# Optimization experiments

Hardware: AMD Instinct MI355X
Metric: run time of the kernel (lower is better)

Reference implementation:

```python
import jax, jax.numpy as jnp
import numpy as np

EPS = 1e-6
MAX_Q = 25.0
B, M, N, S = 1024, 8192, 32, 128


def setup_inputs() -> dict:
    key = jax.random.key(0)
    k = jax.random.split(key, 6)
    z = jax.random.normal(k[0], (B, N), jnp.float32) * 1e-3
    z_j = jax.random.uniform(k[1], (M, N), jnp.float32, -1e-3, 1e-3)
    vec_d_j = jax.random.uniform(k[2], (M, N), jnp.float32, -1e-3, 1e-3)
    T_hat_j = jax.random.uniform(k[3], (M, S), jnp.float32, -1e-3, 1e-3)
    alpha_j = jnp.ones((M,), jnp.float32)
    sigma_par = jax.random.uniform(k[4], (M,), jnp.float32, 0.9, 1.5)
    sigma_perp = jax.random.uniform(k[5], (M,), jnp.float32, 0.1, 0.8)
    return {"z": z, "z_j": z_j, "vec_d_j": vec_d_j, "T_hat_j": T_hat_j,
            "alpha_j": alpha_j, "sigma_par": sigma_par, "sigma_perp": sigma_perp}


def reference(z, z_j, vec_d_j, T_hat_j, alpha_j, sigma_par, sigma_perp):
    tiny = jnp.finfo(sigma_par.dtype).eps
    w_par = 1.0 / jnp.maximum(sigma_par, tiny) ** 2      # [M]
    w_perp = 1.0 / jnp.maximum(sigma_perp, tiny) ** 2    # [M]
    w_diff = w_par - w_perp                               # [M]

    dz = z[:, None, :] - z_j[None, :, :]                  # [B, M, N]
    dz_norm_sq = jnp.sum(dz * dz, axis=-1)                # [B, M]

    d_norm = jnp.linalg.norm(vec_d_j, axis=-1, keepdims=True)  # [M, 1]
    use_proj = (d_norm > EPS).astype(z.dtype)                   # [M, 1]
    b = jnp.where(d_norm > EPS, vec_d_j / d_norm, jnp.zeros_like(vec_d_j))  # [M, N]
    proj = jnp.einsum('bmn,mn->bm', dz, b) * use_proj[:, 0][None, :]        # [B, M]

    q_pos = w_perp[None, :] * dz_norm_sq + w_diff[None, :] * (proj * proj)  # [B, M]
    q_pos = jnp.minimum(q_pos, jnp.asarray(MAX_Q, dtype=z.dtype))

    gain = alpha_j[None, :] * jnp.exp(-jnp.pi * q_pos)    # [B, M]
    T = gain @ T_hat_j                                     # [B, S]
    return T
```

## Files before the change

### kernel.cpp

```cpp
#include <hip/hip_runtime.h>
#include <hip/hip_bf16.h>
#include <math.h>

#define B_SZ 1024
#define M_SZ 8192
#define N_SZ 32
#define S_SZ 128

#define BT     32
#define NTHR   256
#define NSPLIT 16
#define MT     (M_SZ / NSPLIT)
#define MCH    256

#define SG_STRIDE 264

typedef __bf16 bf16x8 __attribute__((ext_vector_type(8)));
typedef float  f32x4  __attribute__((ext_vector_type(4)));

#if defined(__has_builtin)
#if __has_builtin(__builtin_amdgcn_exp2f)
#define EXP2F(x) __builtin_amdgcn_exp2f(x)
#else
#define EXP2F(x) exp2f(x)
#endif
#if __has_builtin(__builtin_amdgcn_rcpf)
#define RCPF(x) __builtin_amdgcn_rcpf(x)
#else
#define RCPF(x) (1.0f / (x))
#endif
#if __has_builtin(__builtin_amdgcn_rsqf)
#define RSQF(x) __builtin_amdgcn_rsqf(x)
#else
#define RSQF(x) (1.0f / sqrtf(x))
#endif
#else
#define EXP2F(x) exp2f(x)
#define RCPF(x) (1.0f / (x))
#define RSQF(x) (1.0f / sqrtf(x))
#endif

#define NEG_PI_LOG2E  (-4.5323601722717285f)
#define E_CLAMP       (-113.30900573730469f)

__global__ __launch_bounds__(NTHR, 2)
void cpsf_one_kernel(const float* __restrict__ z,
                     const float* __restrict__ z_j,
                     const float* __restrict__ vec_d_j,
                     const float* __restrict__ T_hat,
                     const float* __restrict__ alpha_j,
                     const float* __restrict__ sigma_par,
                     const float* __restrict__ sigma_perp,
                     float* __restrict__ out)
{
    __shared__ __align__(16) __bf16 sG[BT * SG_STRIDE];

    const int t     = threadIdx.x;
    const int lane  = t & 63;
    const int w     = t >> 6;
    const int q     = lane >> 4;
    const int c     = lane & 15;
    const int mx    = blockIdx.x;
    const int bbase = blockIdx.y * BT;

    const int wb  = w & 1;
    const int mt0 = (w >> 1) * 8;

    const float* zr = z + (size_t)(bbase + wb*16 + c) * N_SZ + q*8;
    const f32x4 za0 = *(const f32x4*)zr;
    const f32x4 za1 = *(const f32x4*)(zr + 4);
    bf16x8 zA;
    #pragma unroll
    for (int j = 0; j < 4; ++j) { zA[j] = (__bf16)za0[j]; zA[4+j] = (__bf16)za1[j]; }
    float znp = 0.f;
    #pragma unroll
    for (int j = 0; j < 4; ++j) znp += za0[j]*za0[j] + za1[j]*za1[j];
    znp += __shfl_xor(znp, 16);
    znp += __shfl_xor(znp, 32);
    f32x4 zn4;
    #pragma unroll
    for (int reg = 0; reg < 4; ++reg) zn4[reg] = __shfl(znp, q*4 + reg);

    f32x4 acc[2][2];
    #pragma unroll
    for (int bt = 0; bt < 2; ++bt)
        #pragma unroll
        for (int i = 0; i < 2; ++i) acc[bt][i] = (f32x4){0.f,0.f,0.f,0.f};

    const float tiny = 1.1920928955078125e-07f;

    for (int chunk = 0; chunk < MT / MCH; ++chunk) {
        const int m0 = mx * MT + chunk * MCH;

        if (chunk) __syncthreads();

        #pragma unroll 2
        for (int ti = 0; ti < 8; ++ti) {
            const int tile = mt0 + ti;
            const int mg   = m0 + tile*16 + c;
            const float* ar = z_j     + (size_t)mg * N_SZ + q*8;
            const float* dr = vec_d_j + (size_t)mg * N_SZ + q*8;
            const f32x4 a0 = *(const f32x4*)ar;
            const f32x4 a1 = *(const f32x4*)(ar + 4);
            const f32x4 d0 = *(const f32x4*)dr;
            const f32x4 d1 = *(const f32x4*)(dr + 4);

            float zjn = 0.f, dnsq = 0.f, zjd = 0.f;
            #pragma unroll
            for (int j = 0; j < 4; ++j) {
                zjn  += a0[j]*a0[j] + a1[j]*a1[j];
                dnsq += d0[j]*d0[j] + d1[j]*d1[j];
                zjd  += a0[j]*d0[j] + a1[j]*d1[j];
            }
            zjn  += __shfl_xor(zjn, 16);  dnsq += __shfl_xor(dnsq, 16);  zjd += __shfl_xor(zjd, 16);
            zjn  += __shfl_xor(zjn, 32);  dnsq += __shfl_xor(dnsq, 32);  zjd += __shfl_xor(zjd, 32);

            const float inv = (dnsq > 1e-12f) ? RSQF(dnsq) : 0.0f;
            const float sp  = fmaxf(sigma_par[mg],  tiny);
            const float spp = fmaxf(sigma_perp[mg], tiny);
            const float wperp = RCPF(spp * spp);
            const float wpar  = RCPF(sp  * sp);
            const float A  = NEG_PI_LOG2E * wperp;
            const float Cm = A * zjn;
            const float Dm = NEG_PI_LOG2E * (wpar - wperp);
            const float P0 = zjd * inv;
            const float al = alpha_j[mg];

            bf16x8 bz, bd;
            #pragma unroll
            for (int j = 0; j < 4; ++j) {
                bz[j]   = (__bf16)a0[j];        bz[4+j] = (__bf16)a1[j];
                bd[j]   = (__bf16)(d0[j]*inv);  bd[4+j] = (__bf16)(d1[j]*inv);
            }

            f32x4 s1 = __builtin_amdgcn_mfma_f32_16x16x32_bf16(zA, bz, (f32x4){0.f,0.f,0.f,0.f}, 0, 0, 0);
            f32x4 sd = __builtin_amdgcn_mfma_f32_16x16x32_bf16(zA, bd, (f32x4){0.f,0.f,0.f,0.f}, 0, 0, 0);

            #pragma unroll
            for (int reg = 0; reg < 4; ++reg) {
                const float t1 = fmaf(s1[reg], -2.0f, zn4[reg]);
                float e = fmaf(A, t1, Cm);
                const float p = sd[reg] - P0;
                e = fmaf(Dm * p, p, e);
                e = fmaxf(e, E_CLAMP);
                const float g = al * EXP2F(e);
                sG[(size_t)(wb*16 + q*4 + reg) * SG_STRIDE + tile*16 + c] = (__bf16)g;
            }
        }
        __syncthreads();

        #pragma unroll 2
        for (int kc = 0; kc < MCH / 32; ++kc) {
            const float* tp0 = T_hat + (size_t)(m0 + kc*32 + q*8) * S_SZ + (w*2)*16 + c;
            bf16x8 b0, b1;
            #pragma unroll
            for (int j = 0; j < 8; ++j) {
                b0[j] = (__bf16)tp0[(size_t)j * S_SZ];
                b1[j] = (__bf16)tp0[(size_t)j * S_SZ + 16];
            }
            #pragma unroll
            for (int bt = 0; bt < 2; ++bt) {
                const bf16x8 a = *(const bf16x8*)((const char*)sG
                                  + (size_t)(bt*16 + c) * (SG_STRIDE*2) + kc*64 + q*16);
                acc[bt][0] = __builtin_amdgcn_mfma_f32_16x16x32_bf16(a, b0, acc[bt][0], 0, 0, 0);
                acc[bt][1] = __builtin_amdgcn_mfma_f32_16x16x32_bf16(a, b1, acc[bt][1], 0, 0, 0);
            }
        }
    }

    #pragma unroll
    for (int bt = 0; bt < 2; ++bt) {
        float* op = out + (size_t)(bbase + bt*16 + q*4) * S_SZ + w*32 + c;
        #pragma unroll
        for (int i = 0; i < 2; ++i)
            #pragma unroll
            for (int reg = 0; reg < 4; ++reg)
                unsafeAtomicAdd(&op[(size_t)reg * S_SZ + i*16], acc[bt][i][reg]);
    }
}

extern "C" void kernel_launch(void* const* d_in, const int* in_sizes, int n_in,
                              void* d_out, int out_size, void* d_ws, size_t ws_size,
                              hipStream_t stream) {
    (void)in_sizes; (void)n_in; (void)out_size; (void)d_ws; (void)ws_size;

    const float* z          = (const float*)d_in[0];
    const float* z_j        = (const float*)d_in[1];
    const float* vec_d_j    = (const float*)d_in[2];
    const float* T_hat_j    = (const float*)d_in[3];
    const float* alpha_j    = (const float*)d_in[4];
    const float* sigma_par  = (const float*)d_in[5];
    const float* sigma_perp = (const float*)d_in[6];
    float* out = (float*)d_out;

    dim3 grid(NSPLIT, B_SZ / BT);
    cpsf_one_kernel<<<grid, NTHR, 0, stream>>>(
        z, z_j, vec_d_j, T_hat_j, alpha_j, sigma_par, sigma_perp, out);
}
```

Measured before the change: 94.21 us.

## Precompute per-center bf16 operands and swizzled T_hat in a prep kernel

Adds a prep kernel that converts z_j, the normalized vec_d_j and T_hat to bf16 once, in an MFMA-friendly swizzled layout, and stores per-center constants (A, A*|zj|^2, Dm, P0, alpha) in workspace. The main kernel then loads these precomputed operands instead of redoing the norms, reductions, reciprocals and conversions in each of the 32 B-blocks that share an M slice. The goal is to remove redundant per-center work and the strided scalar T_hat loads. The cost is an extra kernel launch and the workspace traffic. The old fused kernel is kept as a fallback when the workspace is too small.

```diff
diff --git a/kernel.cpp b/kernel.cpp
--- a/kernel.cpp
+++ b/kernel.cpp
@@ -43,6 +43,181 @@
 #define NEG_PI_LOG2E  (-4.5323601722717285f)
 #define E_CLAMP       (-113.30900573730469f)
 
+#define WS_TSWZ   ((size_t)0)
+#define WS_ZJBF   ((size_t)2 * 1024 * 1024)
+#define WS_DVBF   (WS_ZJBF + (size_t)M_SZ * N_SZ * 2)
+#define WS_MCONST (WS_DVBF + (size_t)M_SZ * N_SZ * 2)
+#define WS_NEED   (WS_MCONST + (size_t)M_SZ * 8 * 4)
+
+__global__ __launch_bounds__(256)
+void prep_kernel(const float* __restrict__ T,
+                 const float* __restrict__ zj_in,
+                 const float* __restrict__ dv_in,
+                 const float* __restrict__ alpha_j,
+                 const float* __restrict__ sigma_par,
+                 const float* __restrict__ sigma_perp,
+                 char* __restrict__ ws)
+{
+    const int bx = blockIdx.x;
+    const int t  = threadIdx.x;
+
+    if (bx < 512) {
+        const int g    = bx * 256 + t;
+        const int mc   = g >> 9;
+        const int ns   = (g >> 6) & 7;
+        const int lane = g & 63;
+        const int c    = lane & 15;
+        const int q    = lane >> 4;
+        const float* src = T + (size_t)(mc * 32 + q * 8) * S_SZ + ns * 16 + c;
+        bf16x8 v;
+        #pragma unroll
+        for (int j = 0; j < 8; ++j) v[j] = (__bf16)src[(size_t)j * S_SZ];
+        *(bf16x8*)(ws + WS_TSWZ + (size_t)g * 16) = v;
+    } else {
+        const int m = (bx - 512) * 256 + t;
+        float a[N_SZ], d[N_SZ];
+        const float4* a4 = (const float4*)(zj_in + (size_t)m * N_SZ);
+        const float4* d4 = (const float4*)(dv_in + (size_t)m * N_SZ);
+        #pragma unroll
+        for (int i = 0; i < N_SZ / 4; ++i) {
+            float4 av = a4[i], dw = d4[i];
+            a[4*i+0]=av.x; a[4*i+1]=av.y; a[4*i+2]=av.z; a[4*i+3]=av.w;
+            d[4*i+0]=dw.x; d[4*i+1]=dw.y; d[4*i+2]=dw.z; d[4*i+3]=dw.w;
+        }
+        float zjn = 0.f, dnsq = 0.f, zjd = 0.f;
+        #pragma unroll
+        for (int n = 0; n < N_SZ; ++n) {
+            zjn += a[n]*a[n]; dnsq += d[n]*d[n]; zjd += a[n]*d[n];
+        }
+        const float dn  = sqrtf(dnsq);
+        const float inv = (dn > 1e-6f) ? (1.0f / dn) : 0.0f;
+        __bf16* zjb = (__bf16*)(ws + WS_ZJBF) + (size_t)m * N_SZ;
+        __bf16* dvb = (__bf16*)(ws + WS_DVBF) + (size_t)m * N_SZ;
+        #pragma unroll
+        for (int i = 0; i < 4; ++i) {
+            bf16x8 vz, vd;
+            #pragma unroll
+            for (int j = 0; j < 8; ++j) {
+                vz[j] = (__bf16)a[i*8+j];
+                vd[j] = (__bf16)(d[i*8+j] * inv);
+            }
+            *(bf16x8*)(zjb + i*8) = vz;
+            *(bf16x8*)(dvb + i*8) = vd;
+        }
+        const float tiny = 1.1920928955078125e-07f;
+        const float sp  = fmaxf(sigma_par[m],  tiny);
+        const float spp = fmaxf(sigma_perp[m], tiny);
+        const float wperp = 1.0f / (spp * spp);
+        const float wdiff = 1.0f / (sp * sp) - wperp;
+        const float A = NEG_PI_LOG2E * wperp;
+        float* mc8 = (float*)(ws + WS_MCONST) + (size_t)m * 8;
+        *(f32x4*)mc8       = (f32x4){A, A * zjn, NEG_PI_LOG2E * wdiff, zjd * inv};
+        *(f32x4*)(mc8 + 4) = (f32x4){alpha_j[m], 0.f, 0.f, 0.f};
+    }
+}
+
+__global__ __launch_bounds__(NTHR, 2)
+void cpsf_main_kernel(const float* __restrict__ z,
+                      const char* __restrict__ ws_ro,
+                      float* __restrict__ out)
+{
+    __shared__ __align__(16) __bf16 sG[BT * SG_STRIDE];
+
+    const int t     = threadIdx.x;
+    const int lane  = t & 63;
+    const int w     = t >> 6;
+    const int q     = lane >> 4;
+    const int c     = lane & 15;
+    const int mx    = blockIdx.x;
+    const int bbase = blockIdx.y * BT;
+
+    const __bf16* zjbf  = (const __bf16*)(ws_ro + WS_ZJBF);
+    const __bf16* dvbf  = (const __bf16*)(ws_ro + WS_DVBF);
+    const float*  mcst  = (const float*)(ws_ro + WS_MCONST);
+    const char*   Tswz  = ws_ro + WS_TSWZ;
+
+    const int wb  = w & 1;
+    const int mt0 = (w >> 1) * 8;
+
+    const float* zr = z + (size_t)(bbase + wb*16 + c) * N_SZ + q*8;
+    const f32x4 za0 = *(const f32x4*)zr;
+    const f32x4 za1 = *(const f32x4*)(zr + 4);
+    bf16x8 zA;
+    #pragma unroll
+    for (int j = 0; j < 4; ++j) { zA[j] = (__bf16)za0[j]; zA[4+j] = (__bf16)za1[j]; }
+    float znp = 0.f;
+    #pragma unroll
+    for (int j = 0; j < 4; ++j) znp += za0[j]*za0[j] + za1[j]*za1[j];
+    znp += __shfl_xor(znp, 16);
+    znp += __shfl_xor(znp, 32);
+    f32x4 zn4;
+    #pragma unroll
+    for (int reg = 0; reg < 4; ++reg) zn4[reg] = __shfl(znp, q*4 + reg);
+
+    f32x4 acc[2][2];
+    #pragma unroll
+    for (int bt = 0; bt < 2; ++bt)
+        #pragma unroll
+        for (int i = 0; i < 2; ++i) acc[bt][i] = (f32x4){0.f,0.f,0.f,0.f};
+
+    for (int chunk = 0; chunk < MT / MCH; ++chunk) {
+        const int m0 = mx * MT + chunk * MCH;
+
+        if (chunk) __syncthreads();
+
+        #pragma unroll 4
+        for (int ti = 0; ti < 8; ++ti) {
+            const int tile = mt0 + ti;
+            const int mg   = m0 + tile*16 + c;
+            const bf16x8 bz = *(const bf16x8*)(zjbf + (size_t)mg * N_SZ + q*8);
+            const bf16x8 bd = *(const bf16x8*)(dvbf + (size_t)mg * N_SZ + q*8);
+            f32x4 s1 = __builtin_amdgcn_mfma_f32_16x16x32_bf16(zA, bz, (f32x4){0.f,0.f,0.f,0.f}, 0, 0, 0);
+            f32x4 sd = __builtin_amdgcn_mfma_f32_16x16x32_bf16(zA, bd, (f32x4){0.f,0.f,0.f,0.f}, 0, 0, 0);
+            const float* mc8 = mcst + (size_t)mg * 8;
+            const f32x4 mc0 = *(const f32x4*)mc8;
+            const float al  = mc8[4];
+            #pragma unroll
+            for (int reg = 0; reg < 4; ++reg) {
+                const float t1 = fmaf(s1[reg], -2.0f, zn4[reg]);
+                float e = fmaf(mc0[0], t1, mc0[1]);
+                const float p = sd[reg] - mc0[3];
+                e = fmaf(mc0[2] * p, p, e);
+                e = fmaxf(e, E_CLAMP);
+                const float g = al * EXP2F(e);
+                sG[(size_t)(wb*16 + q*4 + reg) * SG_STRIDE + tile*16 + c] = (__bf16)g;
+            }
+        }
+        __syncthreads();
+
+        #pragma unroll
+        for (int kc = 0; kc < MCH / 32; ++kc) {
+            const int mc = mx * (MT/32) + chunk * (MCH/32) + kc;
+            bf16x8 bfr[2];
+            #pragma unroll
+            for (int i = 0; i < 2; ++i)
+                bfr[i] = *(const bf16x8*)(Tswz + ((size_t)(mc*8 + w*2 + i) * 64 + lane) * 16);
+            #pragma unroll
+            for (int bt = 0; bt < 2; ++bt) {
+                const bf16x8 a = *(const bf16x8*)((const char*)sG
+                                  + (size_t)(bt*16 + c) * (SG_STRIDE*2) + kc*64 + q*16);
+                #pragma unroll
+                for (int i = 0; i < 2; ++i)
+                    acc[bt][i] = __builtin_amdgcn_mfma_f32_16x16x32_bf16(a, bfr[i], acc[bt][i], 0, 0, 0);
+            }
+        }
+    }
+
+    #pragma unroll
+    for (int bt = 0; bt < 2; ++bt) {
+        float* op = out + (size_t)(bbase + bt*16 + q*4) * S_SZ + w*32 + c;
+        #pragma unroll
+        for (int i = 0; i < 2; ++i)
+            #pragma unroll
+            for (int reg = 0; reg < 4; ++reg)
+                unsafeAtomicAdd(&op[(size_t)reg * S_SZ + i*16], acc[bt][i][reg]);
+    }
+}
+
 __global__ __launch_bounds__(NTHR, 2)
 void cpsf_one_kernel(const float* __restrict__ z,
                      const float* __restrict__ z_j,
@@ -91,7 +266,6 @@
 
     for (int chunk = 0; chunk < MT / MCH; ++chunk) {
         const int m0 = mx * MT + chunk * MCH;
-
         if (chunk) __syncthreads();
 
         #pragma unroll 2
@@ -182,7 +356,7 @@
 extern "C" void kernel_launch(void* const* d_in, const int* in_sizes, int n_in,
                               void* d_out, int out_size, void* d_ws, size_t ws_size,
                               hipStream_t stream) {
-    (void)in_sizes; (void)n_in; (void)out_size; (void)d_ws; (void)ws_size;
+    (void)in_sizes; (void)n_in; (void)out_size;
 
     const float* z          = (const float*)d_in[0];
     const float* z_j        = (const float*)d_in[1];
@@ -194,6 +368,14 @@
     float* out = (float*)d_out;
 
     dim3 grid(NSPLIT, B_SZ / BT);
-    cpsf_one_kernel<<<grid, NTHR, 0, stream>>>(
-        z, z_j, vec_d_j, T_hat_j, alpha_j, sigma_par, sigma_perp, out);
+
+    if (ws_size >= WS_NEED) {
+        char* ws = (char*)d_ws;
+        prep_kernel<<<dim3(544), 256, 0, stream>>>(
+            T_hat_j, z_j, vec_d_j, alpha_j, sigma_par, sigma_perp, ws);
+        cpsf_main_kernel<<<grid, NTHR, 0, stream>>>(z, ws, out);
+    } else {
+        cpsf_one_kernel<<<grid, NTHR, 0, stream>>>(
+            z, z_j, vec_d_j, T_hat_j, alpha_j, sigma_par, sigma_perp, out);
+    }
 }
```

Measured after the change: 91.62 us. 1.03x faster.
